# Optimization experiments

Measured on AMD Instinct MI355X. Metric: run time of the kernel, lower is better.

Reference implementation:

```python
import jax, jax.numpy as jnp
import numpy as np

D_MODEL = 1024
NUM_HEADS = 16
D_K = D_MODEL // NUM_HEADS
NEG_INF = -1e9


def setup_inputs() -> dict:
    key = jax.random.key(0)
    ks = jax.random.split(key, 12)
    B, S = 2, 2048
    scale = 1.0 / np.sqrt(D_MODEL)
    inp = {
        "q": jax.random.normal(ks[0], (B, S, D_MODEL), jnp.float32),
        "k": jax.random.normal(ks[1], (B, S, D_MODEL), jnp.float32),
        "v": jax.random.normal(ks[2], (B, S, D_MODEL), jnp.float32),
        "mask": jnp.ones((B, S), jnp.int32),
        "W_q": jax.random.normal(ks[3], (D_MODEL, D_MODEL), jnp.float32) * scale,
        "b_q": jnp.zeros((D_MODEL,), jnp.float32),
        "W_k": jax.random.normal(ks[4], (D_MODEL, D_MODEL), jnp.float32) * scale,
        "b_k": jnp.zeros((D_MODEL,), jnp.float32),
        "W_v": jax.random.normal(ks[5], (D_MODEL, D_MODEL), jnp.float32) * scale,
        "b_v": jnp.zeros((D_MODEL,), jnp.float32),
        "W_o": jax.random.normal(ks[6], (D_MODEL, D_MODEL), jnp.float32) * scale,
        "b_o": jnp.zeros((D_MODEL,), jnp.float32),
    }
    return inp


def reference(q, k, v, mask, W_q, b_q, W_k, b_k, W_v, b_v, W_o, b_o):
    B, S, _ = q.shape
    def proj(x, W, b):
        # [B,S,D] -> [B,H,S,d_k]
        y = x @ W.T + b
        return y.reshape(B, -1, NUM_HEADS, D_K).transpose(0, 2, 1, 3)
    qh = proj(q, W_q, b_q)
    kh = proj(k, W_k, b_k)
    vh = proj(v, W_v, b_v)
    scores = jnp.einsum("bhqd,bhkd->bhqk", qh, kh) / jnp.sqrt(jnp.float32(D_K))
    # 2D mask [B,S_k] -> broadcast over heads and query positions
    m = mask[:, None, None, :]
    scores = jnp.where(m == 0, jnp.float32(NEG_INF), scores)
    attn = jax.nn.softmax(scores, axis=-1)
    # dropout is identity at inference
    context = jnp.einsum("bhqk,bhkd->bhqd", attn, vh)
    context = context.transpose(0, 2, 1, 3).reshape(B, S, D_MODEL)
    return context @ W_o.T + b_o
```

## Files before the change

### kernel.cpp

```cpp
#include <hip/hip_runtime.h>
#include <hip/hip_bf16.h>
#include <cstdint>
#include <cstddef>

#define DMODEL 1024
#define NHEADS 16
#define DK 64
#define SEQ 2048
#define BATCH 2
#define NT2 (SEQ / 64)

typedef short bf16x8 __attribute__((ext_vector_type(8)));
typedef float f32x4 __attribute__((ext_vector_type(4)));
typedef float f32x16 __attribute__((ext_vector_type(16)));
typedef unsigned int u32x2 __attribute__((ext_vector_type(2)));
typedef unsigned int u32x4 __attribute__((ext_vector_type(4)));

typedef const __attribute__((address_space(1))) void* gas_ptr;
typedef __attribute__((address_space(3))) void* las_ptr;

__device__ __forceinline__ void gld_lds16(const void* g, void* l) {
    __builtin_amdgcn_global_load_lds((gas_ptr)g, (las_ptr)l, 16, 0, 0);
}

__device__ __forceinline__ ushort f2bf_u(float f) {
    uint32_t x = __float_as_uint(f);
    x += 0x7fff + ((x >> 16) & 1);
    return (ushort)(x >> 16);
}

__global__ __launch_bounds__(256) void cast_all(
        const float* __restrict__ q, const float* __restrict__ k,
        const float* __restrict__ v, const float* __restrict__ Wq,
        const float* __restrict__ Wk, const float* __restrict__ Wv,
        const float* __restrict__ Wo, const int* __restrict__ mask,
        ushort* __restrict__ qb, ushort* __restrict__ kb, ushort* __restrict__ vb,
        ushort* __restrict__ Wqb, ushort* __restrict__ Wkb,
        ushort* __restrict__ Wvb, ushort* __restrict__ Wob,
        float* __restrict__ mb) {
    int bid = blockIdx.x;
    if (bid >= 16384) {
        int i = (bid - 16384) * 1024 + threadIdx.x * 4;
        int4 mk = *reinterpret_cast<const int4*>(mask + i);
        float4 o;
        o.x = mk.x ? 0.f : -1e9f;
        o.y = mk.y ? 0.f : -1e9f;
        o.z = mk.z ? 0.f : -1e9f;
        o.w = mk.w ? 0.f : -1e9f;
        *reinterpret_cast<float4*>(mb + i) = o;
        return;
    }
    const float* src; ushort* dst; int base;
    if      (bid <  4096) { src = q;  dst = qb;  base = bid; }
    else if (bid <  8192) { src = k;  dst = kb;  base = bid - 4096; }
    else if (bid < 12288) { src = v;  dst = vb;  base = bid - 8192; }
    else if (bid < 13312) { src = Wq; dst = Wqb; base = bid - 12288; }
    else if (bid < 14336) { src = Wk; dst = Wkb; base = bid - 13312; }
    else if (bid < 15360) { src = Wv; dst = Wvb; base = bid - 14336; }
    else                  { src = Wo; dst = Wob; base = bid - 15360; }
    int i = base * 1024 + threadIdx.x * 4;
    float4 f = *reinterpret_cast<const float4*>(src + i);
    ushort4 o;
    o.x = f2bf_u(f.x); o.y = f2bf_u(f.y); o.z = f2bf_u(f.z); o.w = f2bf_u(f.w);
    *reinterpret_cast<ushort4*>(dst + i) = o;
}

__global__ __launch_bounds__(256) void gemm_qkv(
        const ushort* __restrict__ A,
        const ushort* __restrict__ Wall,
        const float* __restrict__ bq, const float* __restrict__ bk,
        const float* __restrict__ bv,
        ushort* __restrict__ Qh, ushort* __restrict__ Kh, ushort* __restrict__ Vt) {
    __shared__ ushort As[128 * 64];
    __shared__ ushort Bs[128 * 64];
    const int tid = threadIdx.x;
    const int w = tid >> 6, lane = tid & 63;
    const int lr = lane & 15, lg = lane >> 4;
    int lid = (blockIdx.x & 7) * 96 + (blockIdx.x >> 3);
    const int tMg = (lid >> 3) << 7;
    const int tN  = (lid & 7) << 7;
    const int g   = tMg >> 12;
    const ushort* W = Wall + (size_t)g * 1024 * 1024;
    const float* bias = (g == 0) ? bq : (g == 1 ? bk : bv);
    const int wr = (w >> 1) * 64, wc = (w & 1) * 64;

    f32x4 acc[4][4] = {};

    const ushort* gAsrc[4];
    const ushort* gBsrc[4];
#pragma unroll
    for (int i = 0; i < 4; i++) {
        int slot = (w * 4 + i) * 64 + lane;
        int row = slot >> 3, sr = slot & 7;
        int cd = sr ^ (row & 7);
        gAsrc[i] = A + (size_t)(tMg + row) * 1024 + cd * 8;
        gBsrc[i] = W + (size_t)(tN + row) * 1024 + cd * 8;
    }

    for (int k0 = 0; k0 < 1024; k0 += 64) {
#pragma unroll
        for (int i = 0; i < 4; i++)
            gld_lds16(gAsrc[i] + k0, As + (w * 4 + i) * 512);
#pragma unroll
        for (int i = 0; i < 4; i++)
            gld_lds16(gBsrc[i] + k0, Bs + (w * 4 + i) * 512);
        __syncthreads();

#pragma unroll
        for (int ks = 0; ks < 2; ks++) {
            bf16x8 af[4], bfr[4];
#pragma unroll
            for (int i = 0; i < 4; i++)
                af[i] = *(const bf16x8*)(As + (wr + i * 16 + lr) * 64 +
                                         (((ks * 4 + lg) ^ (lr & 7)) * 8));
#pragma unroll
            for (int i = 0; i < 4; i++)
                bfr[i] = *(const bf16x8*)(Bs + (wc + i * 16 + lr) * 64 +
                                          (((ks * 4 + lg) ^ (lr & 7)) * 8));
#pragma unroll
            for (int mi = 0; mi < 4; mi++)
#pragma unroll
                for (int ni = 0; ni < 4; ni++)
                    acc[mi][ni] = __builtin_amdgcn_mfma_f32_16x16x32_bf16(
                        af[mi], bfr[ni], acc[mi][ni], 0, 0, 0);
        }
        __syncthreads();
    }

#pragma unroll
    for (int mi = 0; mi < 4; mi++) {
        const int row0 = tMg + wr + mi * 16 + lg * 4;
#pragma unroll
        for (int ni = 0; ni < 4; ni++) {
            const int col = tN + wc + ni * 16 + lr;
            const int h = col >> 6, d = col & (DK - 1);
            const float bvv = bias[col];
            if (g == 2) {
                int mloc = row0 & 4095;
                int b = mloc >> 11, s0 = mloc & (SEQ - 1);
                ushort4 o4;
                o4.x = f2bf_u(acc[mi][ni][0] + bvv);
                o4.y = f2bf_u(acc[mi][ni][1] + bvv);
                o4.z = f2bf_u(acc[mi][ni][2] + bvv);
                o4.w = f2bf_u(acc[mi][ni][3] + bvv);
                *reinterpret_cast<ushort4*>(
                    &Vt[(((size_t)(b * NHEADS + h) * DK + d) * SEQ) + s0]) = o4;
            } else {
#pragma unroll
                for (int r = 0; r < 4; r++) {
                    float vv = acc[mi][ni][r] + bvv;
                    int mloc = (row0 + r) & 4095;
                    int b = mloc >> 11, s = mloc & (SEQ - 1);
                    if (g == 0)
                        Qh[(((size_t)(b * NHEADS + h) * SEQ + s) * DK) + d] = f2bf_u(vv);
                    else
                        Kh[(((size_t)(b * NHEADS + h) * SEQ + s) * DK) + d] = f2bf_u(vv);
                }
            }
        }
    }
}

__global__ __launch_bounds__(256) void gemm_out(
        const ushort* __restrict__ A,
        const ushort* __restrict__ W,
        const float* __restrict__ bias,
        float* __restrict__ out, int M, int N, int K) {
    __shared__ ushort As[64 * 64];
    __shared__ ushort Bs[128 * 64];
    const int tid = threadIdx.x;
    const int w = tid >> 6, lane = tid & 63;
    const int lr = lane & 15, lg = lane >> 4;
    const int nTiles = N >> 7;
    const int cpx = gridDim.x >> 3;
    int lid = (blockIdx.x & 7) * cpx + (blockIdx.x >> 3);
    const int tM = (lid / nTiles) << 6;
    const int tN = (lid % nTiles) << 7;
    const int wr = (w >> 1) * 32, wc = (w & 1) * 64;

    f32x4 acc[2][4] = {};

    const ushort* gAsrc[2];
    const ushort* gBsrc[4];
#pragma unroll
    for (int i = 0; i < 2; i++) {
        int slot = (w * 2 + i) * 64 + lane;
        int row = slot >> 3, sr = slot & 7;
        int cd = sr ^ (row & 7);
        gAsrc[i] = A + (size_t)(tM + row) * K + cd * 8;
    }
#pragma unroll
    for (int i = 0; i < 4; i++) {
        int slot = (w * 4 + i) * 64 + lane;
        int row = slot >> 3, sr = slot & 7;
        int cd = sr ^ (row & 7);
        gBsrc[i] = W + (size_t)(tN + row) * K + cd * 8;
    }

    for (int k0 = 0; k0 < K; k0 += 64) {
#pragma unroll
        for (int i = 0; i < 2; i++)
            gld_lds16(gAsrc[i] + k0, As + (w * 2 + i) * 512);
#pragma unroll
        for (int i = 0; i < 4; i++)
            gld_lds16(gBsrc[i] + k0, Bs + (w * 4 + i) * 512);
        __syncthreads();

#pragma unroll
        for (int ks = 0; ks < 2; ks++) {
            bf16x8 af[2], bfr[4];
#pragma unroll
            for (int i = 0; i < 2; i++)
                af[i] = *(const bf16x8*)(As + (wr + i * 16 + lr) * 64 +
                                         (((ks * 4 + lg) ^ (lr & 7)) * 8));
#pragma unroll
            for (int i = 0; i < 4; i++)
                bfr[i] = *(const bf16x8*)(Bs + (wc + i * 16 + lr) * 64 +
                                          (((ks * 4 + lg) ^ (lr & 7)) * 8));
#pragma unroll
            for (int mi = 0; mi < 2; mi++)
#pragma unroll
                for (int ni = 0; ni < 4; ni++)
                    acc[mi][ni] = __builtin_amdgcn_mfma_f32_16x16x32_bf16(
                        af[mi], bfr[ni], acc[mi][ni], 0, 0, 0);
        }
        __syncthreads();
    }

#pragma unroll
    for (int mi = 0; mi < 2; mi++) {
        const int row0 = tM + wr + mi * 16 + lg * 4;
#pragma unroll
        for (int ni = 0; ni < 4; ni++) {
            const int col = tN + wc + ni * 16 + lr;
            const float bv = bias[col];
#pragma unroll
            for (int r = 0; r < 4; r++)
                out[(size_t)(row0 + r) * N + col] = acc[mi][ni][r] + bv;
        }
    }
}

#define SCALE2 0.18033688011120542f

__device__ __forceinline__ bf16x8 pack_pa(const float* p) {
    uint a, b, c, d;
    asm("v_cvt_pk_bf16_f32 %0, %1, %2" : "=v"(a) : "v"(p[0]), "v"(p[1]));
    asm("v_cvt_pk_bf16_f32 %0, %1, %2" : "=v"(b) : "v"(p[4]), "v"(p[5]));
    asm("v_cvt_pk_bf16_f32 %0, %1, %2" : "=v"(c) : "v"(p[2]), "v"(p[3]));
    asm("v_cvt_pk_bf16_f32 %0, %1, %2" : "=v"(d) : "v"(p[6]), "v"(p[7]));
    asm("v_permlane32_swap_b32 %0, %1" : "+v"(a), "+v"(b));
    asm("v_permlane32_swap_b32 %0, %1" : "+v"(c), "+v"(d));
    union { u32x4 u; bf16x8 h; } cv;
    cv.u = (u32x4){a, c, b, d};
    return cv.h;
}

__global__ __launch_bounds__(256) void attn_fwd32(
        const ushort* __restrict__ Qh, const ushort* __restrict__ Kh,
        const ushort* __restrict__ Vt, const float* __restrict__ mbias,
        ushort* __restrict__ ctx) {
    __shared__ ushort Ks[2][2][2048];
    __shared__ ushort Vs[2][2][2048];
    __shared__ float  Ml[SEQ];

    const int tid = threadIdx.x;
    const int w = tid >> 6;
    const int l = tid & 63;
    const int q32 = l & 31, hi = l >> 5;
    const int q7 = l & 7;

    int lid = (blockIdx.x & 7) * 64 + (blockIdx.x >> 3);
    const int qblk = lid & 15;
    const int bh = lid >> 4;
    const int b = bh >> 4;
    const int h = bh & 15;
    const int q0 = qblk * 128 + w * 32;

    const ushort* Qp = Qh + (size_t)bh * SEQ * DK + (size_t)(q0 + q32) * DK + hi * 8;
    const ushort* Kg = Kh + (size_t)bh * SEQ * DK;
    const ushort* Vg = Vt + (size_t)bh * DK * SEQ;

    const int srow = tid >> 3;
    const int scs  = (tid & 7) ^ (srow & 7);
    const ushort* Ksrc = Kg + (size_t)srow * DK + scs * 8;
    const ushort* Vsrc = Vg + (size_t)(srow + ((scs & 4) << 3)) * SEQ + (scs & 3) * 8;

    {
        const float* mg = mbias + (size_t)b * SEQ;
        gld_lds16(mg + tid * 4,        &Ml[w * 256]);
        gld_lds16(mg + 1024 + tid * 4, &Ml[1024 + w * 256]);
    }

    auto STAGE = [&](int buf, int t) {
        const int kv0 = t * 64;
        gld_lds16(Ksrc + (size_t)kv0 * DK,        &Ks[buf][0][w * 512]);
        gld_lds16(Ksrc + (size_t)(kv0 + 32) * DK, &Ks[buf][1][w * 512]);
        gld_lds16(Vsrc + kv0,                     &Vs[buf][0][w * 512]);
        gld_lds16(Vsrc + kv0 + 32,                &Vs[buf][1][w * 512]);
    };

    bf16x8 qf[4];
#pragma unroll
    for (int dc = 0; dc < 4; dc++)
        qf[dc] = *(const bf16x8*)(Qp + dc * 16);

    const short one_s = (short)0x3F80;
    const bf16x8 ones = {one_s, one_s, one_s, one_s, one_s, one_s, one_s, one_s};

    f32x16 c0 = {}, c1 = {};
    f32x16 lacc = {};

    STAGE(0, 0);
    __syncthreads();

    for (int t = 0; t < NT2; ++t) {
        const int buf = t & 1;
        if (t + 1 < NT2) STAGE(buf ^ 1, t + 1);

        const int kv0 = t * 64;

        bf16x8 kf0[4], kf1[4];
#pragma unroll
        for (int dc = 0; dc < 4; dc++)
            kf0[dc] = *(const bf16x8*)(&Ks[buf][0][q32 * 64 + (((dc * 2 + hi) ^ q7) * 8)]);
        f32x16 s0 = {}, s1 = {};
        __builtin_amdgcn_s_setprio(1);
#pragma unroll
        for (int dc = 0; dc < 4; dc++)
            s0 = __builtin_amdgcn_mfma_f32_32x32x16_bf16(kf0[dc], qf[dc], s0, 0, 0, 0);
        __builtin_amdgcn_s_setprio(0);
#pragma unroll
        for (int dc = 0; dc < 4; dc++)
            kf1[dc] = *(const bf16x8*)(&Ks[buf][1][q32 * 64 + (((dc * 2 + hi) ^ q7) * 8)]);
        __builtin_amdgcn_s_setprio(1);
#pragma unroll
        for (int dc = 0; dc < 4; dc++)
            s1 = __builtin_amdgcn_mfma_f32_32x32x16_bf16(kf1[dc], qf[dc], s1, 0, 0, 0);
        __builtin_amdgcn_s_setprio(0);

        float e0[16];
#pragma unroll
        for (int g = 0; g < 4; g++) {
            float4 mb0 = *reinterpret_cast<const float4*>(&Ml[kv0 + g * 8 + hi * 4]);
#pragma unroll
            for (int j = 0; j < 4; j++)
                e0[g * 4 + j] = __builtin_amdgcn_exp2f(
                    fmaf(s0[g * 4 + j], SCALE2, reinterpret_cast<const float*>(&mb0)[j]));
        }
        bf16x8 pa00 = pack_pa(e0);
        bf16x8 pa01 = pack_pa(e0 + 8);
        bf16x8 vc0[4];
#pragma unroll
        for (int dt = 0; dt < 2; dt++)
#pragma unroll
            for (int ks = 0; ks < 2; ks++)
                vc0[dt * 2 + ks] = *(const bf16x8*)(&Vs[buf][0][q32 * 64 + (((dt * 4 + ks * 2 + hi) ^ q7) * 8)]);
        __builtin_amdgcn_s_setprio(1);
        c0 = __builtin_amdgcn_mfma_f32_32x32x16_bf16(pa00, vc0[0], c0, 0, 0, 0);
        c1 = __builtin_amdgcn_mfma_f32_32x32x16_bf16(pa00, vc0[2], c1, 0, 0, 0);
        c0 = __builtin_amdgcn_mfma_f32_32x32x16_bf16(pa01, vc0[1], c0, 0, 0, 0);
        c1 = __builtin_amdgcn_mfma_f32_32x32x16_bf16(pa01, vc0[3], c1, 0, 0, 0);
        lacc = __builtin_amdgcn_mfma_f32_32x32x16_bf16(pa00, ones, lacc, 0, 0, 0);
        lacc = __builtin_amdgcn_mfma_f32_32x32x16_bf16(pa01, ones, lacc, 0, 0, 0);
        __builtin_amdgcn_s_setprio(0);

        float e1[16];
#pragma unroll
        for (int g = 0; g < 4; g++) {
            float4 mb1 = *reinterpret_cast<const float4*>(&Ml[kv0 + 32 + g * 8 + hi * 4]);
#pragma unroll
            for (int j = 0; j < 4; j++)
                e1[g * 4 + j] = __builtin_amdgcn_exp2f(
                    fmaf(s1[g * 4 + j], SCALE2, reinterpret_cast<const float*>(&mb1)[j]));
        }
        bf16x8 pa10 = pack_pa(e1);
        bf16x8 pa11 = pack_pa(e1 + 8);
        bf16x8 vc1[4];
#pragma unroll
        for (int dt = 0; dt < 2; dt++)
#pragma unroll
            for (int ks = 0; ks < 2; ks++)
                vc1[dt * 2 + ks] = *(const bf16x8*)(&Vs[buf][1][q32 * 64 + (((dt * 4 + ks * 2 + hi) ^ q7) * 8)]);
        __builtin_amdgcn_s_setprio(1);
        c0 = __builtin_amdgcn_mfma_f32_32x32x16_bf16(pa10, vc1[0], c0, 0, 0, 0);
        c1 = __builtin_amdgcn_mfma_f32_32x32x16_bf16(pa10, vc1[2], c1, 0, 0, 0);
        c0 = __builtin_amdgcn_mfma_f32_32x32x16_bf16(pa11, vc1[1], c0, 0, 0, 0);
        c1 = __builtin_amdgcn_mfma_f32_32x32x16_bf16(pa11, vc1[3], c1, 0, 0, 0);
        lacc = __builtin_amdgcn_mfma_f32_32x32x16_bf16(pa10, ones, lacc, 0, 0, 0);
        lacc = __builtin_amdgcn_mfma_f32_32x32x16_bf16(pa11, ones, lacc, 0, 0, 0);
        __builtin_amdgcn_s_setprio(0);

        __syncthreads();
    }

#pragma unroll
    for (int r = 0; r < 16; r++) {
        int crow = (r & 3) + 8 * (r >> 2) + 4 * hi;
        float rlT = __builtin_amdgcn_rcpf(lacc[r]);
        int qq = q0 + crow;
        size_t base = (size_t)(b * SEQ + qq) * DMODEL + h * DK;
        ctx[base + q32]      = f2bf_u(c0[r] * rlT);
        ctx[base + 32 + q32] = f2bf_u(c1[r] * rlT);
    }
}

extern "C" void kernel_launch(void* const* d_in, const int* in_sizes, int n_in,
                              void* d_out, int out_size, void* d_ws, size_t ws_size,
                              hipStream_t stream) {
    const float* q    = (const float*)d_in[0];
    const float* k    = (const float*)d_in[1];
    const float* v    = (const float*)d_in[2];
    const int*   mask = (const int*)d_in[3];
    const float* Wq   = (const float*)d_in[4];
    const float* bq   = (const float*)d_in[5];
    const float* Wk   = (const float*)d_in[6];
    const float* bk   = (const float*)d_in[7];
    const float* Wv   = (const float*)d_in[8];
    const float* bv   = (const float*)d_in[9];
    const float* Wo   = (const float*)d_in[10];
    const float* bo   = (const float*)d_in[11];

    char* ws = (char*)d_ws;
    ushort* qb   = (ushort*)(ws + (size_t)0);
    ushort* kb   = (ushort*)(ws + ((size_t)8  << 20));
    ushort* vb   = (ushort*)(ws + ((size_t)16 << 20));
    ushort* Wqb  = (ushort*)(ws + ((size_t)24 << 20));
    ushort* Wkb  = (ushort*)(ws + ((size_t)26 << 20));
    ushort* Wvb  = (ushort*)(ws + ((size_t)28 << 20));
    ushort* Wob  = (ushort*)(ws + ((size_t)30 << 20));
    ushort* Qh   = (ushort*)(ws + ((size_t)32 << 20));
    ushort* Kh   = (ushort*)(ws + ((size_t)40 << 20));
    ushort* Vt   = (ushort*)(ws + ((size_t)48 << 20));
    ushort* ctxb = (ushort*)(ws + ((size_t)56 << 20));
    float*  mbias = (float*)d_out;

    cast_all<<<16388, 256, 0, stream>>>(q, k, v, Wq, Wk, Wv, Wo, mask,
                                        qb, kb, vb, Wqb, Wkb, Wvb, Wob, mbias);

    gemm_qkv<<<768, 256, 0, stream>>>(qb, Wqb, bq, bk, bv, Qh, Kh, Vt);

    attn_fwd32<<<BATCH * NHEADS * (SEQ / 128), 256, 0, stream>>>(Qh, Kh, Vt, mbias, ctxb);

    const int M = BATCH * SEQ;
    gemm_out<<<(M / 64) * (DMODEL / 128), 256, 0, stream>>>(
        ctxb, Wob, bo, (float*)d_out, M, DMODEL, DMODEL);
}
```

Before: 131.4 us.

## Give each wave private K/V staging to drop block barriers in attention loop

Each wave now loads its own copy of the K/V tiles into a per-wave LDS region, 32 keys per step with double buffering, and uses vmcnt/lgkmcnt waits instead of __syncthreads. This removes block-wide barriers and lets waves run independently. The cost is that every wave re-fetches the same K/V from global/L2, giving four times the load traffic and four times the LDS footprint. Per-iteration work is halved, so there are more loop iterations.

Measured after the change: 140.2 us. 1.07x slower.

```diff
diff --git a/kernel.cpp b/kernel.cpp
--- a/kernel.cpp
+++ b/kernel.cpp
@@ -8,7 +8,7 @@
 #define DK 64
 #define SEQ 2048
 #define BATCH 2
-#define NT2 (SEQ / 64)
+#define NT (SEQ / 32)
 
 typedef short bf16x8 __attribute__((ext_vector_type(8)));
 typedef float f32x4 __attribute__((ext_vector_type(4)));
@@ -260,8 +260,8 @@
         const ushort* __restrict__ Qh, const ushort* __restrict__ Kh,
         const ushort* __restrict__ Vt, const float* __restrict__ mbias,
         ushort* __restrict__ ctx) {
-    __shared__ ushort Ks[2][2][2048];
-    __shared__ ushort Vs[2][2][2048];
+    __shared__ ushort Ks[4][2][2048];
+    __shared__ ushort Vs[4][2][2048];
     __shared__ float  Ml[SEQ];
 
     const int tid = threadIdx.x;
@@ -281,10 +281,20 @@
     const ushort* Kg = Kh + (size_t)bh * SEQ * DK;
     const ushort* Vg = Vt + (size_t)bh * DK * SEQ;
 
-    const int srow = tid >> 3;
-    const int scs  = (tid & 7) ^ (srow & 7);
-    const ushort* Ksrc = Kg + (size_t)srow * DK + scs * 8;
-    const ushort* Vsrc = Vg + (size_t)(srow + ((scs & 4) << 3)) * SEQ + (scs & 3) * 8;
+    const int lrow = l >> 3;
+    const int cd   = (l & 7) ^ lrow;
+    const ushort* Ksrc = Kg + (size_t)lrow * DK + cd * 8;
+    const ushort* Vsrc = Vg + (size_t)(lrow + ((cd & 4) << 3)) * SEQ + (cd & 3) * 8;
+
+    auto STAGE = [&](int buf, int t) {
+        const int kv0 = t * 32;
+#pragma unroll
+        for (int i = 0; i < 4; i++)
+            gld_lds16(Ksrc + (size_t)(kv0 + i * 8) * DK, &Ks[w][buf][i * 512]);
+#pragma unroll
+        for (int i = 0; i < 4; i++)
+            gld_lds16(Vsrc + (size_t)(i * 8) * SEQ + kv0, &Vs[w][buf][i * 512]);
+    };
 
     {
         const float* mg = mbias + (size_t)b * SEQ;
@@ -292,14 +302,6 @@
         gld_lds16(mg + 1024 + tid * 4, &Ml[1024 + w * 256]);
     }
 
-    auto STAGE = [&](int buf, int t) {
-        const int kv0 = t * 64;
-        gld_lds16(Ksrc + (size_t)kv0 * DK,        &Ks[buf][0][w * 512]);
-        gld_lds16(Ksrc + (size_t)(kv0 + 32) * DK, &Ks[buf][1][w * 512]);
-        gld_lds16(Vsrc + kv0,                     &Vs[buf][0][w * 512]);
-        gld_lds16(Vsrc + kv0 + 32,                &Vs[buf][1][w * 512]);
-    };
-
     bf16x8 qf[4];
 #pragma unroll
     for (int dc = 0; dc < 4; dc++)
@@ -312,86 +314,63 @@
     f32x16 lacc = {};
 
     STAGE(0, 0);
+    STAGE(1, 1);
     __syncthreads();
 
-    for (int t = 0; t < NT2; ++t) {
+    for (int t = 0; t < NT; ++t) {
         const int buf = t & 1;
-        if (t + 1 < NT2) STAGE(buf ^ 1, t + 1);
-
-        const int kv0 = t * 64;
-
-        bf16x8 kf0[4], kf1[4];
+
+        if (t < NT - 1) asm volatile("s_waitcnt vmcnt(8)" ::: "memory");
+        else            asm volatile("s_waitcnt vmcnt(0)" ::: "memory");
+        __builtin_amdgcn_sched_barrier(0);
+
+        const int kv0 = t * 32;
+        bf16x8 kf[4];
 #pragma unroll
         for (int dc = 0; dc < 4; dc++)
-            kf0[dc] = *(const bf16x8*)(&Ks[buf][0][q32 * 64 + (((dc * 2 + hi) ^ q7) * 8)]);
-        f32x16 s0 = {}, s1 = {};
+            kf[dc] = *(const bf16x8*)(&Ks[w][buf][q32 * 64 + (((dc * 2 + hi) ^ q7) * 8)]);
+        bf16x8 vc[4];
+#pragma unroll
+        for (int dt = 0; dt < 2; dt++)
+#pragma unroll
+            for (int ks = 0; ks < 2; ks++)
+                vc[dt * 2 + ks] = *(const bf16x8*)(&Vs[w][buf][q32 * 64 + (((dt * 4 + ks * 2 + hi) ^ q7) * 8)]);
+        float4 mb0 = *reinterpret_cast<const float4*>(&Ml[kv0 + hi * 4]);
+        float4 mb1 = *reinterpret_cast<const float4*>(&Ml[kv0 + 8 + hi * 4]);
+        float4 mb2 = *reinterpret_cast<const float4*>(&Ml[kv0 + 16 + hi * 4]);
+        float4 mb3 = *reinterpret_cast<const float4*>(&Ml[kv0 + 24 + hi * 4]);
+
+        asm volatile("s_waitcnt lgkmcnt(0)" ::: "memory");
+        __builtin_amdgcn_sched_barrier(0);
+        if (t + 2 < NT) STAGE(buf, t + 2);
+
+        f32x16 s = {};
         __builtin_amdgcn_s_setprio(1);
 #pragma unroll
         for (int dc = 0; dc < 4; dc++)
-            s0 = __builtin_amdgcn_mfma_f32_32x32x16_bf16(kf0[dc], qf[dc], s0, 0, 0, 0);
+            s = __builtin_amdgcn_mfma_f32_32x32x16_bf16(kf[dc], qf[dc], s, 0, 0, 0);
         __builtin_amdgcn_s_setprio(0);
-#pragma unroll
-        for (int dc = 0; dc < 4; dc++)
-            kf1[dc] = *(const bf16x8*)(&Ks[buf][1][q32 * 64 + (((dc * 2 + hi) ^ q7) * 8)]);
+
+        float e[16];
+        const float* mbp[4] = {(const float*)&mb0, (const float*)&mb1,
+                               (const float*)&mb2, (const float*)&mb3};
+#pragma unroll
+        for (int g = 0; g < 4; g++)
+#pragma unroll
+            for (int j = 0; j < 4; j++)
+                e[g * 4 + j] = __builtin_amdgcn_exp2f(
+                    fmaf(s[g * 4 + j], SCALE2, mbp[g][j]));
+        bf16x8 pa0 = pack_pa(e);
+        bf16x8 pa1 = pack_pa(e + 8);
+
         __builtin_amdgcn_s_setprio(1);
-#pragma unroll
-        for (int dc = 0; dc < 4; dc++)
-            s1 = __builtin_amdgcn_mfma_f32_32x32x16_bf16(kf1[dc], qf[dc], s1, 0, 0, 0);
+        c0 = __builtin_amdgcn_mfma_f32_32x32x16_bf16(pa0, vc[0], c0, 0, 0, 0);
+        c1 = __builtin_amdgcn_mfma_f32_32x32x16_bf16(pa0, vc[2], c1, 0, 0, 0);
+        c0 = __builtin_amdgcn_mfma_f32_32x32x16_bf16(pa1, vc[1], c0, 0, 0, 0);
+        c1 = __builtin_amdgcn_mfma_f32_32x32x16_bf16(pa1, vc[3], c1, 0, 0, 0);
+        lacc = __builtin_amdgcn_mfma_f32_32x32x16_bf16(pa0, ones, lacc, 0, 0, 0);
+        lacc = __builtin_amdgcn_mfma_f32_32x32x16_bf16(pa1, ones, lacc, 0, 0, 0);
         __builtin_amdgcn_s_setprio(0);
-
-        float e0[16];
-#pragma unroll
-        for (int g = 0; g < 4; g++) {
-            float4 mb0 = *reinterpret_cast<const float4*>(&Ml[kv0 + g * 8 + hi * 4]);
-#pragma unroll
-            for (int j = 0; j < 4; j++)
-                e0[g * 4 + j] = __builtin_amdgcn_exp2f(
-                    fmaf(s0[g * 4 + j], SCALE2, reinterpret_cast<const float*>(&mb0)[j]));
-        }
-        bf16x8 pa00 = pack_pa(e0);
-        bf16x8 pa01 = pack_pa(e0 + 8);
-        bf16x8 vc0[4];
-#pragma unroll
-        for (int dt = 0; dt < 2; dt++)
-#pragma unroll
-            for (int ks = 0; ks < 2; ks++)
-                vc0[dt * 2 + ks] = *(const bf16x8*)(&Vs[buf][0][q32 * 64 + (((dt * 4 + ks * 2 + hi) ^ q7) * 8)]);
-        __builtin_amdgcn_s_setprio(1);
-        c0 = __builtin_amdgcn_mfma_f32_32x32x16_bf16(pa00, vc0[0], c0, 0, 0, 0);
-        c1 = __builtin_amdgcn_mfma_f32_32x32x16_bf16(pa00, vc0[2], c1, 0, 0, 0);
-        c0 = __builtin_amdgcn_mfma_f32_32x32x16_bf16(pa01, vc0[1], c0, 0, 0, 0);
-        c1 = __builtin_amdgcn_mfma_f32_32x32x16_bf16(pa01, vc0[3], c1, 0, 0, 0);
-        lacc = __builtin_amdgcn_mfma_f32_32x32x16_bf16(pa00, ones, lacc, 0, 0, 0);
-        lacc = __builtin_amdgcn_mfma_f32_32x32x16_bf16(pa01, ones, lacc, 0, 0, 0);
-        __builtin_amdgcn_s_setprio(0);
-
-        float e1[16];
-#pragma unroll
-        for (int g = 0; g < 4; g++) {
-            float4 mb1 = *reinterpret_cast<const float4*>(&Ml[kv0 + 32 + g * 8 + hi * 4]);
-#pragma unroll
-            for (int j = 0; j < 4; j++)
-                e1[g * 4 + j] = __builtin_amdgcn_exp2f(
-                    fmaf(s1[g * 4 + j], SCALE2, reinterpret_cast<const float*>(&mb1)[j]));
-        }
-        bf16x8 pa10 = pack_pa(e1);
-        bf16x8 pa11 = pack_pa(e1 + 8);
-        bf16x8 vc1[4];
-#pragma unroll
-        for (int dt = 0; dt < 2; dt++)
-#pragma unroll
-            for (int ks = 0; ks < 2; ks++)
-                vc1[dt * 2 + ks] = *(const bf16x8*)(&Vs[buf][1][q32 * 64 + (((dt * 4 + ks * 2 + hi) ^ q7) * 8)]);
-        __builtin_amdgcn_s_setprio(1);
-        c0 = __builtin_amdgcn_mfma_f32_32x32x16_bf16(pa10, vc1[0], c0, 0, 0, 0);
-        c1 = __builtin_amdgcn_mfma_f32_32x32x16_bf16(pa10, vc1[2], c1, 0, 0, 0);
-        c0 = __builtin_amdgcn_mfma_f32_32x32x16_bf16(pa11, vc1[1], c0, 0, 0, 0);
-        c1 = __builtin_amdgcn_mfma_f32_32x32x16_bf16(pa11, vc1[3], c1, 0, 0, 0);
-        lacc = __builtin_amdgcn_mfma_f32_32x32x16_bf16(pa10, ones, lacc, 0, 0, 0);
-        lacc = __builtin_amdgcn_mfma_f32_32x32x16_bf16(pa11, ones, lacc, 0, 0, 0);
-        __builtin_amdgcn_s_setprio(0);
-
-        __syncthreads();
     }
 
 #pragma unroll
```
